# Kernel optimization log

Measured on AMD Instinct MI355X. Metric: run time of the kernel, lower is better.

Reference implementation:

```python
import jax, jax.numpy as jnp
import numpy as np

N, NFEAT, NHID, NCLASS, NHEAD = 8192, 512, 64, 16, 4
ALPHA = 0.1  # leaky relu slope
NEG = -9e15


def setup_inputs() -> dict:
    key = jax.random.key(0)
    ks = jax.random.split(key, 7)
    x = jax.random.normal(ks[0], (N, NFEAT), dtype=jnp.float32)
    adj = (jax.random.uniform(ks[1], (N, N)) < 0.05).astype(jnp.float32)
    # per-head params: W [H, nfeat, nhid], a [H, 2*nhid] (xavier-ish scale)
    W = jax.random.normal(ks[2], (NHEAD, NFEAT, NHID), dtype=jnp.float32) * (1.0 / np.sqrt(NFEAT))
    a = jax.random.normal(ks[3], (NHEAD, 2 * NHID), dtype=jnp.float32) * (1.0 / np.sqrt(NHID))
    W_out = jax.random.normal(ks[4], (NHEAD * NHID, NCLASS), dtype=jnp.float32) * (1.0 / np.sqrt(NHEAD * NHID))
    a_out = jax.random.normal(ks[5], (2 * NCLASS,), dtype=jnp.float32) * (1.0 / np.sqrt(NCLASS))
    return {"x": x, "adj": adj, "W": W, "a": a, "W_out": W_out, "a_out": a_out}


def _gat_layer(h, adj, Wk, ak):
    """Dense pyGAT GraphAttentionLayer (eval mode, dropout = identity)."""
    d = Wk.shape[1]
    Wh = h @ Wk                         # [N, d]
    f1 = Wh @ ak[:d]                    # [N]
    f2 = Wh @ ak[d:]                    # [N]
    e = jax.nn.leaky_relu(f1[:, None] + f2[None, :], negative_slope=ALPHA)  # [N, N]
    att = jax.nn.softmax(jnp.where(adj > 0, e, NEG), axis=1)
    return att @ Wh                     # [N, d]


def reference(x, adj, W, a, W_out, a_out):
    # eval mode: F.dropout is identity
    heads = jax.vmap(lambda Wk, ak: jax.nn.elu(_gat_layer(x, adj, Wk, ak)))(W, a)  # [H, N, nhid]
    h = jnp.transpose(heads, (1, 0, 2)).reshape(x.shape[0], -1)                    # [N, H*nhid]
    out = jax.nn.elu(_gat_layer(h, adj, W_out, a_out))                             # [N, nclass]
    return jax.nn.log_softmax(out, axis=1)
```

## Files before the change

kernel.cpp:

```cpp
#include <hip/hip_runtime.h>
#include <hip/hip_bf16.h>

#define NN 8192
#define NFEAT 512
#define NHID 64
#define NCLASS 16
#define NHEAD 4
#define ALPHA 0.1f
#define CAP 768

typedef short bf16x8 __attribute__((ext_vector_type(8)));
typedef float f32x4 __attribute__((ext_vector_type(4)));
typedef float fv4 __attribute__((ext_vector_type(4)));

__device__ __forceinline__ float lrelu(float x) { return fmaxf(x, ALPHA * x); }
__device__ __forceinline__ float elu(float x) { return x > 0.f ? x : __expf(x) - 1.f; }
__device__ __forceinline__ short f2b(float x) {
  union { __bf16 b; short s; } c; c.b = (__bf16)x; return c.s;
}
__device__ __forceinline__ float b2f(short x) {
  union { unsigned int u; float f; } c; c.u = ((unsigned int)(unsigned short)x) << 16; return c.f;
}

#define UPF(w, v, A0, A1)                                  \
  {                                                        \
    const float lo_ = __uint_as_float((v) << 16);          \
    const float hi_ = __uint_as_float((v) & 0xffff0000u);  \
    (A0) += (w) * lo_;                                     \
    (A1) += (w) * hi_;                                     \
  }

__global__ __launch_bounds__(256) void k_wprep(const float* __restrict__ W,
                                               short* __restrict__ WB) {
  __shared__ float t[64][65];
  const int h = blockIdx.y;
  const int k0 = blockIdx.x * 64;
  const int tid = threadIdx.x;
#pragma unroll
  for (int it = 0; it < 16; ++it) {
    const int r = it * 4 + (tid >> 6), c = tid & 63;
    t[r][c] = W[((size_t)h * NFEAT + k0 + r) * NHID + c];
  }
  __syncthreads();
#pragma unroll
  for (int it = 0; it < 16; ++it) {
    const int d = it * 4 + (tid >> 6), k = tid & 63;
    WB[((size_t)h * NHID + d) * NFEAT + k0 + k] = f2b(t[k][d]);
  }
}

__global__ __launch_bounds__(256) void k_prep1(const float* __restrict__ x,
                                               const short* __restrict__ WB,
                                               const float* __restrict__ a,
                                               short* __restrict__ WhB2,
                                               float* __restrict__ f1i,
                                               float* __restrict__ f2i) {
  __shared__ short tile[64][72];
  const int bid = blockIdx.x;
  const int h = bid >> 7;
  const int bm = (bid & 127) * 64;
  const int tid = threadIdx.x;
  const int wv = tid >> 6, lane = tid & 63;
  const int mr = lane & 15, kg = lane >> 4;
  f32x4 acc0 = {0.f, 0.f, 0.f, 0.f}, acc1 = acc0, acc2 = acc0, acc3 = acc0;
  const float* ap = x + (size_t)(bm + wv * 16 + mr) * NFEAT + kg * 8;
  const short* bp = WB + ((size_t)h * NHID + mr) * NFEAT + kg * 8;
#pragma unroll 2
  for (int k0 = 0; k0 < NFEAT; k0 += 32) {
    const float4 xa = *reinterpret_cast<const float4*>(ap);
    const float4 xb = *reinterpret_cast<const float4*>(ap + 4);
    bf16x8 af;
    af[0] = f2b(xa.x); af[1] = f2b(xa.y); af[2] = f2b(xa.z); af[3] = f2b(xa.w);
    af[4] = f2b(xb.x); af[5] = f2b(xb.y); af[6] = f2b(xb.z); af[7] = f2b(xb.w);
    const bf16x8 b0 = *reinterpret_cast<const bf16x8*>(bp);
    const bf16x8 b1 = *reinterpret_cast<const bf16x8*>(bp + 16 * NFEAT);
    const bf16x8 b2 = *reinterpret_cast<const bf16x8*>(bp + 32 * NFEAT);
    const bf16x8 b3 = *reinterpret_cast<const bf16x8*>(bp + 48 * NFEAT);
    acc0 = __builtin_amdgcn_mfma_f32_16x16x32_bf16(af, b0, acc0, 0, 0, 0);
    acc1 = __builtin_amdgcn_mfma_f32_16x16x32_bf16(af, b1, acc1, 0, 0, 0);
    acc2 = __builtin_amdgcn_mfma_f32_16x16x32_bf16(af, b2, acc2, 0, 0, 0);
    acc3 = __builtin_amdgcn_mfma_f32_16x16x32_bf16(af, b3, acc3, 0, 0, 0);
    ap += 32; bp += 32;
  }
  float a1v[4], a2v[4];
#pragma unroll
  for (int c = 0; c < 4; ++c) {
    a1v[c] = a[h * 128 + mr + c * 16];
    a2v[c] = a[h * 128 + 64 + mr + c * 16];
  }
#pragma unroll
  for (int q = 0; q < 4; ++q) {
    float s1 = acc0[q] * a1v[0] + acc1[q] * a1v[1] + acc2[q] * a1v[2] + acc3[q] * a1v[3];
    float s2 = acc0[q] * a2v[0] + acc1[q] * a2v[1] + acc2[q] * a2v[2] + acc3[q] * a2v[3];
#pragma unroll
    for (int off = 1; off < 16; off <<= 1) {
      s1 += __shfl_xor(s1, off);
      s2 += __shfl_xor(s2, off);
    }
    if (mr == 0) {
      const int i = bm + wv * 16 + kg * 4 + q;
      f1i[(size_t)i * 4 + h] = s1;
      f2i[(size_t)i * 4 + h] = s2;
    }
  }
#pragma unroll
  for (int q = 0; q < 4; ++q) {
    const int r = wv * 16 + kg * 4 + q;
    tile[r][mr +  0] = f2b(acc0[q]);
    tile[r][mr + 16] = f2b(acc1[q]);
    tile[r][mr + 32] = f2b(acc2[q]);
    tile[r][mr + 48] = f2b(acc3[q]);
  }
  __syncthreads();
  {
    const int row = tid >> 2, seg = tid & 3;
    bf16x8 o0, o1;
#pragma unroll
    for (int u = 0; u < 8; ++u) {
      o0[u] = tile[row][seg * 16 + u];
      o1[u] = tile[row][seg * 16 + 8 + u];
    }
    short* dst = WhB2 + (size_t)(h >> 1) * NN * 128 + (size_t)(bm + row) * 128 +
                 (h & 1) * 64 + seg * 16;
    *reinterpret_cast<bf16x8*>(dst) = o0;
    *reinterpret_cast<bf16x8*>(dst + 8) = o1;
  }
}

__global__ __launch_bounds__(256) void k_rmax(const float* __restrict__ src,
                                              float* __restrict__ dst, int n, int stride,
                                              int boff) {
  const float* p = src + (size_t)blockIdx.x * boff;
  float m = -1e30f;
  for (int k = threadIdx.x; k < n; k += 256) m = fmaxf(m, p[(size_t)k * stride]);
#pragma unroll
  for (int off = 32; off; off >>= 1) m = fmaxf(m, __shfl_xor(m, off));
  __shared__ float sm[4];
  if ((threadIdx.x & 63) == 0) sm[threadIdx.x >> 6] = m;
  __syncthreads();
  if (threadIdx.x == 0) dst[blockIdx.x] = fmaxf(fmaxf(sm[0], sm[1]), fmaxf(sm[2], sm[3]));
}

__global__ __launch_bounds__(256) void k_scan(const float* __restrict__ adj,
                                              unsigned int* __restrict__ bmask) {
  const fv4* a4 = reinterpret_cast<const fv4*>(adj);
  const int t0 = blockIdx.x * 256 + threadIdx.x;
#pragma unroll 4
  for (int it = 0; it < 32; ++it) {
    const int g = it * 524288 + t0;
    const fv4 v = __builtin_nontemporal_load(a4 + g);
    unsigned int nv = (unsigned int)((v.x > 0.f) | ((v.y > 0.f) << 1) |
                                     ((v.z > 0.f) << 2) | ((v.w > 0.f) << 3))
                      << ((threadIdx.x & 7) * 4);
    nv |= __shfl_xor(nv, 1);
    nv |= __shfl_xor(nv, 2);
    nv |= __shfl_xor(nv, 4);
    if ((threadIdx.x & 7) == 0) bmask[g >> 3] = nv;
  }
}

__global__ __launch_bounds__(256) void k_attn1h(const unsigned int* __restrict__ bmask,
                                                const short* __restrict__ WhB2,
                                                const float* __restrict__ f1i,
                                                const float* __restrict__ f2i,
                                                const float* __restrict__ f2max,
                                                short* __restrict__ hcat) {
  __shared__ unsigned short idx[CAP];
  __shared__ unsigned int widx[2][CAP + 32];
  __shared__ float red[4][64];
  __shared__ float swred[4][2];
  __shared__ float sinv[2];
  __shared__ int cnt;
  const int i = blockIdx.x;
  const int p = blockIdx.y;
  const int tid = threadIdx.x;
  const int wv = tid >> 6, lane = tid & 63;
  if (tid == 0) cnt = 0;
  __syncthreads();

  {
    unsigned int word = bmask[(size_t)i * 256 + tid];
    const int c = __popc(word);
    if (c) {
      int base = atomicAdd(&cnt, c);
      const int j0 = tid * 32;
      while (word) {
        const int b = __ffs(word) - 1;
        word &= word - 1;
        if (base < CAP) idx[base++] = (unsigned short)(j0 + b);
      }
    }
  }
  __syncthreads();
  const int n = min(cnt, CAP);

  if (tid < 64) widx[tid >> 5][n + (tid & 31)] = 0;

  const float f1r0 = f1i[(size_t)i * 4 + p * 2];
  const float f1r1 = f1i[(size_t)i * 4 + p * 2 + 1];
  const float mrow0 = lrelu(f1r0 + f2max[p * 2]);
  const float mrow1 = lrelu(f1r1 + f2max[p * 2 + 1]);
  float sw0 = 0.f, sw1 = 0.f;
  for (int k = tid; k < n; k += 256) {
    const int j = idx[k];
    const float2 f = *reinterpret_cast<const float2*>(f2i + (size_t)j * 4 + p * 2);
    const float w0 = __expf(lrelu(f1r0 + f.x) - mrow0);
    const float w1 = __expf(lrelu(f1r1 + f.y) - mrow1);
    widx[0][k] = ((unsigned int)(unsigned short)f2b(w0) << 16) | (unsigned int)j;
    widx[1][k] = ((unsigned int)(unsigned short)f2b(w1) << 16) | (unsigned int)j;
    sw0 += w0; sw1 += w1;
  }
#pragma unroll
  for (int off = 32; off; off >>= 1) { sw0 += __shfl_xor(sw0, off); sw1 += __shfl_xor(sw1, off); }
  if (lane == 0) { swred[wv][0] = sw0; swred[wv][1] = sw1; }
  __syncthreads();
  if (tid < 2) sinv[tid] = 1.f / (swred[0][tid] + swred[1][tid] + swred[2][tid] + swred[3][tid]);

  const int hl = wv >> 1, half = wv & 1;
  const int grp = lane >> 4, l = lane & 15;
  float acc0 = 0.f, acc1 = 0.f, acc2 = 0.f, acc3 = 0.f;
  const short* wb = WhB2 + (size_t)p * NN * 128 + hl * 64 + l * 4;
  const unsigned int* wrow = widx[hl];
  __syncthreads();
  for (int kb = (half * 4 + grp) * 8; kb < n; kb += 64) {
    const uint4 pa = *reinterpret_cast<const uint4*>(wrow + kb);
    const uint4 pb = *reinterpret_cast<const uint4*>(wrow + kb + 4);
    const uint2 e0 = *reinterpret_cast<const uint2*>(wb + (size_t)(pa.x & 0xffffu) * 128);
    const uint2 e1 = *reinterpret_cast<const uint2*>(wb + (size_t)(pa.y & 0xffffu) * 128);
    const uint2 e2 = *reinterpret_cast<const uint2*>(wb + (size_t)(pa.z & 0xffffu) * 128);
    const uint2 e3 = *reinterpret_cast<const uint2*>(wb + (size_t)(pa.w & 0xffffu) * 128);
    const uint2 e4 = *reinterpret_cast<const uint2*>(wb + (size_t)(pb.x & 0xffffu) * 128);
    const uint2 e5 = *reinterpret_cast<const uint2*>(wb + (size_t)(pb.y & 0xffffu) * 128);
    const uint2 e6 = *reinterpret_cast<const uint2*>(wb + (size_t)(pb.z & 0xffffu) * 128);
    const uint2 e7 = *reinterpret_cast<const uint2*>(wb + (size_t)(pb.w & 0xffffu) * 128);
    const float w0 = __uint_as_float(pa.x & 0xffff0000u);
    const float w1 = __uint_as_float(pa.y & 0xffff0000u);
    const float w2 = __uint_as_float(pa.z & 0xffff0000u);
    const float w3 = __uint_as_float(pa.w & 0xffff0000u);
    const float w4 = __uint_as_float(pb.x & 0xffff0000u);
    const float w5 = __uint_as_float(pb.y & 0xffff0000u);
    const float w6 = __uint_as_float(pb.z & 0xffff0000u);
    const float w7 = __uint_as_float(pb.w & 0xffff0000u);
    UPF(w0, e0.x, acc0, acc1) UPF(w0, e0.y, acc2, acc3)
    UPF(w1, e1.x, acc0, acc1) UPF(w1, e1.y, acc2, acc3)
    UPF(w2, e2.x, acc0, acc1) UPF(w2, e2.y, acc2, acc3)
    UPF(w3, e3.x, acc0, acc1) UPF(w3, e3.y, acc2, acc3)
    UPF(w4, e4.x, acc0, acc1) UPF(w4, e4.y, acc2, acc3)
    UPF(w5, e5.x, acc0, acc1) UPF(w5, e5.y, acc2, acc3)
    UPF(w6, e6.x, acc0, acc1) UPF(w6, e6.y, acc2, acc3)
    UPF(w7, e7.x, acc0, acc1) UPF(w7, e7.y, acc2, acc3)
  }
  acc0 += __shfl_xor(acc0, 16); acc0 += __shfl_xor(acc0, 32);
  acc1 += __shfl_xor(acc1, 16); acc1 += __shfl_xor(acc1, 32);
  acc2 += __shfl_xor(acc2, 16); acc2 += __shfl_xor(acc2, 32);
  acc3 += __shfl_xor(acc3, 16); acc3 += __shfl_xor(acc3, 32);
  if (lane < 16) {
    red[wv][l * 4 + 0] = acc0;
    red[wv][l * 4 + 1] = acc1;
    red[wv][l * 4 + 2] = acc2;
    red[wv][l * 4 + 3] = acc3;
  }
  __syncthreads();
  if (tid < 128) {
    const int sub = tid >> 6, d = tid & 63;
    const float s = red[sub * 2][d] + red[sub * 2 + 1][d];
    hcat[(size_t)i * 256 + p * 128 + sub * 64 + d] = f2b(elu(s * sinv[sub]));
  }
}

__global__ __launch_bounds__(256) void k_gemm2(const short* __restrict__ hcat,
                                               const float* __restrict__ Wout,
                                               const float* __restrict__ aout,
                                               short* __restrict__ Wh2B,
                                               float* __restrict__ f1o,
                                               float* __restrict__ f2o) {
  __shared__ float sW[NHEAD * NHID][NCLASS + 1];
  __shared__ float sh[16][NHEAD * NHID + 1];
  const int tid = threadIdx.x;
  const int r = tid >> 4, c = tid & 15;
  const int row = blockIdx.x * 16 + r;
  for (int u = tid; u < 256 * 16; u += 256) sW[u >> 4][u & 15] = Wout[u];
  for (int u = tid; u < 16 * 256; u += 256)
    sh[u >> 8][u & 255] = b2f(hcat[(size_t)(blockIdx.x * 16 + (u >> 8)) * 256 + (u & 255)]);
  __syncthreads();
  float acc = 0.f;
#pragma unroll 8
  for (int f = 0; f < 256; ++f) acc += sh[r][f] * sW[f][c];
  Wh2B[(size_t)row * NCLASS + c] = f2b(acc);
  float s1 = acc * aout[c];
  float s2 = acc * aout[NCLASS + c];
#pragma unroll
  for (int off = 8; off; off >>= 1) { s1 += __shfl_xor(s1, off); s2 += __shfl_xor(s2, off); }
  if (c == 0) { f1o[row] = s1; f2o[row] = s2; }
}

__global__ __launch_bounds__(256) void k_attn2(const unsigned int* __restrict__ bmask,
                                               const short* __restrict__ Wh2B,
                                               const float* __restrict__ f1o,
                                               const float* __restrict__ f2o,
                                               const float* __restrict__ f2omax,
                                               float* __restrict__ out) {
  __shared__ unsigned short idx[CAP];
  __shared__ unsigned int wj[CAP + 4];
  __shared__ float red[4][NCLASS];
  __shared__ float swp[4];
  __shared__ float sinvs;
  __shared__ int cnt;
  const int i = blockIdx.x;
  const int tid = threadIdx.x;
  const int wv = tid >> 6, lane = tid & 63;
  if (tid == 0) cnt = 0;
  __syncthreads();

  {
    unsigned int word = bmask[(size_t)i * 256 + tid];
    const int c = __popc(word);
    if (c) {
      int base = atomicAdd(&cnt, c);
      const int j0 = tid * 32;
      while (word) {
        const int b = __ffs(word) - 1;
        word &= word - 1;
        if (base < CAP) idx[base++] = (unsigned short)(j0 + b);
      }
    }
  }
  __syncthreads();
  const int n = min(cnt, CAP);
  if (tid < 4) wj[n + tid] = 0;

  const float f1r = f1o[i];
  const float mrow = lrelu(f1r + f2omax[0]);
  float sw = 0.f;
  for (int k = tid; k < n; k += 256) {
    const int j = idx[k];
    const float w = __expf(lrelu(f1r + f2o[j]) - mrow);
    wj[k] = ((unsigned int)(unsigned short)f2b(w) << 16) | (unsigned int)j;
    sw += w;
  }
#pragma unroll
  for (int off = 32; off; off >>= 1) sw += __shfl_xor(sw, off);
  if (lane == 0) swp[wv] = sw;
  __syncthreads();
  if (tid == 0) sinvs = 1.f / (swp[0] + swp[1] + swp[2] + swp[3]);
  __syncthreads();

  const int grp = tid >> 2, gl = tid & 3;
  float acc0 = 0.f, acc1 = 0.f, acc2 = 0.f, acc3 = 0.f;
  const short* wb = Wh2B + gl * 4;
  for (int kb = grp * 4; kb < n; kb += 256) {
    const uint4 pw = *reinterpret_cast<const uint4*>(wj + kb);
    const uint2 e0 = *reinterpret_cast<const uint2*>(wb + (size_t)(pw.x & 0xffffu) * NCLASS);
    const uint2 e1 = *reinterpret_cast<const uint2*>(wb + (size_t)(pw.y & 0xffffu) * NCLASS);
    const uint2 e2 = *reinterpret_cast<const uint2*>(wb + (size_t)(pw.z & 0xffffu) * NCLASS);
    const uint2 e3 = *reinterpret_cast<const uint2*>(wb + (size_t)(pw.w & 0xffffu) * NCLASS);
    const float w0 = __uint_as_float(pw.x & 0xffff0000u);
    const float w1 = __uint_as_float(pw.y & 0xffff0000u);
    const float w2 = __uint_as_float(pw.z & 0xffff0000u);
    const float w3 = __uint_as_float(pw.w & 0xffff0000u);
    UPF(w0, e0.x, acc0, acc1) UPF(w0, e0.y, acc2, acc3)
    UPF(w1, e1.x, acc0, acc1) UPF(w1, e1.y, acc2, acc3)
    UPF(w2, e2.x, acc0, acc1) UPF(w2, e2.y, acc2, acc3)
    UPF(w3, e3.x, acc0, acc1) UPF(w3, e3.y, acc2, acc3)
  }
  acc0 += __shfl_xor(acc0, 4);  acc1 += __shfl_xor(acc1, 4);
  acc2 += __shfl_xor(acc2, 4);  acc3 += __shfl_xor(acc3, 4);
  acc0 += __shfl_xor(acc0, 8);  acc1 += __shfl_xor(acc1, 8);
  acc2 += __shfl_xor(acc2, 8);  acc3 += __shfl_xor(acc3, 8);
  acc0 += __shfl_xor(acc0, 16); acc1 += __shfl_xor(acc1, 16);
  acc2 += __shfl_xor(acc2, 16); acc3 += __shfl_xor(acc3, 16);
  acc0 += __shfl_xor(acc0, 32); acc1 += __shfl_xor(acc1, 32);
  acc2 += __shfl_xor(acc2, 32); acc3 += __shfl_xor(acc3, 32);
  if (lane < 4) {
    red[wv][lane * 4 + 0] = acc0;
    red[wv][lane * 4 + 1] = acc1;
    red[wv][lane * 4 + 2] = acc2;
    red[wv][lane * 4 + 3] = acc3;
  }
  __syncthreads();
  if (tid < NCLASS) {
    const float s = red[0][tid] + red[1][tid] + red[2][tid] + red[3][tid];
    const float v = elu(s * sinvs);
    float vm = v;
#pragma unroll
    for (int off = 8; off; off >>= 1) vm = fmaxf(vm, __shfl_xor(vm, off, 16));
    float ex = __expf(v - vm);
#pragma unroll
    for (int off = 8; off; off >>= 1) ex += __shfl_xor(ex, off, 16);
    out[(size_t)i * NCLASS + tid] = v - vm - __logf(ex);
  }
}

extern "C" void kernel_launch(void* const* d_in, const int* in_sizes, int n_in,
                              void* d_out, int out_size, void* d_ws, size_t ws_size,
                              hipStream_t stream) {
  const float* x    = (const float*)d_in[0];
  const float* adj  = (const float*)d_in[1];
  const float* W    = (const float*)d_in[2];
  const float* a    = (const float*)d_in[3];
  const float* Wout = (const float*)d_in[4];
  const float* aout = (const float*)d_in[5];
  float* out = (float*)d_out;
  char* ws = (char*)d_ws;
  const size_t MB = 1048576;

  unsigned int* bmask  = (unsigned int*)(ws);
  short* WhB2          = (short*)(ws + 8 * MB);
  short* hcat          = (short*)(ws + 12 * MB);
  short* WB            = (short*)(ws + 16 * MB);
  float* f1i           = (float*)(ws + 16 * MB + 262144);
  float* f2i           = (float*)(ws + 16 * MB + 393216);
  float* f1o           = (float*)(ws + 16 * MB + 524288);
  float* f2o           = (float*)(ws + 16 * MB + 557056);
  short* Wh2B          = (short*)(ws + 16 * MB + 589824);
  float* f2max         = (float*)(ws + 16 * MB + 851968);
  float* f2omax        = (float*)(ws + 16 * MB + 852032);

  k_wprep<<<dim3(8, 4), 256, 0, stream>>>(W, WB);
  k_prep1<<<512, 256, 0, stream>>>(x, WB, a, WhB2, f1i, f2i);
  k_rmax<<<NHEAD, 256, 0, stream>>>(f2i, f2max, NN, 4, 1);
  k_scan<<<2048, 256, 0, stream>>>(adj, bmask);
  k_attn1h<<<dim3(NN, 2), 256, 0, stream>>>(bmask, WhB2, f1i, f2i, f2max, hcat);
  k_gemm2<<<NN / 16, 256, 0, stream>>>(hcat, Wout, aout, Wh2B, f1o, f2o);
  k_rmax<<<1, 256, 0, stream>>>(f2o, f2omax, NN, 1, 0);
  k_attn2<<<NN, 256, 0, stream>>>(bmask, Wh2B, f1o, f2o, f2omax, out);
}
```

Measured before the change: 247.2 us.

## Replace sparse gather attention with dense masked MFMA over 64-row tiles

The first-layer attention no longer compacts neighbour indices per row and gathers Wh rows. It now runs a dense masked bf16 MFMA over all 8192 columns for 64-row tiles per head. The leaky-relu exponential is factored as max(A*B, C*D) using per-row and per-column precomputed exponentials from a new k_acbd kernel, so the inner loop has no transcendentals. Wh is stored in a column-blocked layout that fits the MFMA B operand. This trades irregular gathers and per-row scan work for about 20x more (mostly zero-weight) dense FLOPs on matrix cores, and the factored exponentials may lose precision for extreme values.

```diff
diff --git a/kernel.cpp b/kernel.cpp
--- a/kernel.cpp
+++ b/kernel.cpp
@@ -52,7 +52,7 @@
 __global__ __launch_bounds__(256) void k_prep1(const float* __restrict__ x,
                                                const short* __restrict__ WB,
                                                const float* __restrict__ a,
-                                               short* __restrict__ WhB2,
+                                               short* __restrict__ Whf,
                                                float* __restrict__ f1i,
                                                float* __restrict__ f2i) {
   __shared__ short tile[64][72];
@@ -112,18 +112,15 @@
     tile[r][mr + 48] = f2b(acc3[q]);
   }
   __syncthreads();
-  {
-    const int row = tid >> 2, seg = tid & 3;
-    bf16x8 o0, o1;
-#pragma unroll
-    for (int u = 0; u < 8; ++u) {
-      o0[u] = tile[row][seg * 16 + u];
-      o1[u] = tile[row][seg * 16 + 8 + u];
-    }
-    short* dst = WhB2 + (size_t)(h >> 1) * NN * 128 + (size_t)(bm + row) * 128 +
-                 (h & 1) * 64 + seg * 16;
-    *reinterpret_cast<bf16x8*>(dst) = o0;
-    *reinterpret_cast<bf16x8*>(dst + 8) = o1;
+#pragma unroll
+  for (int it = 0; it < 2; ++it) {
+    const int jbl = (tid >> 6) + it * 4;
+    const int d = tid & 63;
+    bf16x8 o;
+#pragma unroll
+    for (int jo = 0; jo < 8; ++jo) o[jo] = tile[jbl * 8 + jo][d];
+    *reinterpret_cast<bf16x8*>(Whf +
+        (((size_t)h * 1024 + (bm >> 3) + jbl) * 64 + d) * 8) = o;
   }
 }
 
@@ -139,6 +136,29 @@
   if ((threadIdx.x & 63) == 0) sm[threadIdx.x >> 6] = m;
   __syncthreads();
   if (threadIdx.x == 0) dst[blockIdx.x] = fmaxf(fmaxf(sm[0], sm[1]), fmaxf(sm[2], sm[3]));
+}
+
+__global__ __launch_bounds__(256) void k_acbd(const float* __restrict__ f1i,
+                                              const float* __restrict__ f2i,
+                                              const float* __restrict__ f2max,
+                                              float2* __restrict__ ACh,
+                                              unsigned int* __restrict__ BDh) {
+  const int idx = blockIdx.x * 256 + threadIdx.x;
+  const int i = idx & (NN - 1);
+  const int h = idx >> 13;
+  const float fm = f2max[h];
+  const float f1 = f1i[(size_t)i * 4 + h];
+  const float f2 = f2i[(size_t)i * 4 + h];
+  const float s = f1 + fm;
+  const float mrow = fmaxf(s, 0.1f * s);
+  float2 ac;
+  ac.x = __expf(s - mrow);
+  ac.y = __expf(0.1f * s - mrow);
+  ACh[(size_t)h * NN + i] = ac;
+  const float t = f2 - fm;
+  const unsigned int B = (unsigned short)f2b(__expf(t));
+  const unsigned int D = (unsigned short)f2b(__expf(0.1f * t));
+  BDh[(size_t)h * NN + i] = B | (D << 16);
 }
 
 __global__ __launch_bounds__(256) void k_scan(const float* __restrict__ adj,
@@ -159,112 +179,92 @@
   }
 }
 
-__global__ __launch_bounds__(256) void k_attn1h(const unsigned int* __restrict__ bmask,
-                                                const short* __restrict__ WhB2,
-                                                const float* __restrict__ f1i,
-                                                const float* __restrict__ f2i,
-                                                const float* __restrict__ f2max,
+#define DCH 512
+__global__ __launch_bounds__(256) void k_dense1(const unsigned int* __restrict__ bmask,
+                                                const short* __restrict__ Whf,
+                                                const float2* __restrict__ ACh,
+                                                const unsigned int* __restrict__ BDh,
                                                 short* __restrict__ hcat) {
-  __shared__ unsigned short idx[CAP];
-  __shared__ unsigned int widx[2][CAP + 32];
-  __shared__ float red[4][64];
-  __shared__ float swred[4][2];
-  __shared__ float sinv[2];
-  __shared__ int cnt;
-  const int i = blockIdx.x;
-  const int p = blockIdx.y;
+  __shared__ unsigned int sm_mask[64][16];
+  __shared__ unsigned int sm_bd[DCH];
+  __shared__ float sm_iv[4][16];
+  __shared__ short sm_out[64][72];
+  const int i0 = blockIdx.x * 64;
+  const int h = blockIdx.y;
   const int tid = threadIdx.x;
   const int wv = tid >> 6, lane = tid & 63;
-  if (tid == 0) cnt = 0;
-  __syncthreads();
-
+  const int mr = lane & 15, kg = lane >> 4;
+  const int row_local = wv * 16 + mr;
+  const float2 ac = ACh[(size_t)h * NN + i0 + row_local];
+  f32x4 acc0 = {0.f, 0.f, 0.f, 0.f}, acc1 = acc0, acc2 = acc0, acc3 = acc0;
+  float rs = 0.f;
+  const int rr = tid >> 2, w0 = (tid & 3) * 4;
+
+  for (int jc = 0; jc < NN; jc += DCH) {
+    __syncthreads();
+    {
+      const unsigned int* src = bmask + (size_t)(i0 + rr) * 256 + (jc >> 5);
+#pragma unroll
+      for (int u = 0; u < 4; ++u) sm_mask[rr][w0 + u] = src[w0 + u];
+      sm_bd[tid] = BDh[(size_t)h * NN + jc + tid];
+      sm_bd[tid + 256] = BDh[(size_t)h * NN + jc + tid + 256];
+    }
+    __syncthreads();
+#pragma unroll 4
+    for (int ks = 0; ks < DCH / 32; ++ks) {
+      const int jl = ks * 32 + kg * 8;
+      const uint4 bda = *reinterpret_cast<const uint4*>(&sm_bd[jl]);
+      const uint4 bdb = *reinterpret_cast<const uint4*>(&sm_bd[jl + 4]);
+      const unsigned int mb = (sm_mask[row_local][ks] >> (kg * 8)) & 0xffu;
+      bf16x8 af;
+#define MKW(e, bdw)                                              \
+      {                                                          \
+        const float Bf = __uint_as_float((bdw) << 16);           \
+        const float Df = __uint_as_float((bdw) & 0xffff0000u);   \
+        float w_ = fmaxf(ac.x * Bf, ac.y * Df);                  \
+        w_ = ((mb >> (e)) & 1u) ? w_ : 0.f;                      \
+        rs += w_;                                                \
+        af[e] = f2b(w_);                                         \
+      }
+      MKW(0, bda.x) MKW(1, bda.y) MKW(2, bda.z) MKW(3, bda.w)
+      MKW(4, bdb.x) MKW(5, bdb.y) MKW(6, bdb.z) MKW(7, bdb.w)
+#undef MKW
+      const short* wp = Whf + (((size_t)h * 1024 + ((jc + jl) >> 3)) * 64 + mr) * 8;
+      const bf16x8 bf0 = *reinterpret_cast<const bf16x8*>(wp);
+      const bf16x8 bf1 = *reinterpret_cast<const bf16x8*>(wp + 128);
+      const bf16x8 bf2 = *reinterpret_cast<const bf16x8*>(wp + 256);
+      const bf16x8 bf3 = *reinterpret_cast<const bf16x8*>(wp + 384);
+      acc0 = __builtin_amdgcn_mfma_f32_16x16x32_bf16(af, bf0, acc0, 0, 0, 0);
+      acc1 = __builtin_amdgcn_mfma_f32_16x16x32_bf16(af, bf1, acc1, 0, 0, 0);
+      acc2 = __builtin_amdgcn_mfma_f32_16x16x32_bf16(af, bf2, acc2, 0, 0, 0);
+      acc3 = __builtin_amdgcn_mfma_f32_16x16x32_bf16(af, bf3, acc3, 0, 0, 0);
+    }
+  }
+  rs += __shfl_xor(rs, 16);
+  rs += __shfl_xor(rs, 32);
+  if (lane < 16) sm_iv[wv][lane] = 1.f / rs;
+  __syncthreads();
+#pragma unroll
+  for (int q = 0; q < 4; ++q) {
+    const float ivq = sm_iv[wv][kg * 4 + q];
+    const int r = wv * 16 + kg * 4 + q;
+    sm_out[r][mr +  0] = f2b(elu(acc0[q] * ivq));
+    sm_out[r][mr + 16] = f2b(elu(acc1[q] * ivq));
+    sm_out[r][mr + 32] = f2b(elu(acc2[q] * ivq));
+    sm_out[r][mr + 48] = f2b(elu(acc3[q] * ivq));
+  }
+  __syncthreads();
   {
-    unsigned int word = bmask[(size_t)i * 256 + tid];
-    const int c = __popc(word);
-    if (c) {
-      int base = atomicAdd(&cnt, c);
-      const int j0 = tid * 32;
-      while (word) {
-        const int b = __ffs(word) - 1;
-        word &= word - 1;
-        if (base < CAP) idx[base++] = (unsigned short)(j0 + b);
-      }
-    }
-  }
-  __syncthreads();
-  const int n = min(cnt, CAP);
-
-  if (tid < 64) widx[tid >> 5][n + (tid & 31)] = 0;
-
-  const float f1r0 = f1i[(size_t)i * 4 + p * 2];
-  const float f1r1 = f1i[(size_t)i * 4 + p * 2 + 1];
-  const float mrow0 = lrelu(f1r0 + f2max[p * 2]);
-  const float mrow1 = lrelu(f1r1 + f2max[p * 2 + 1]);
-  float sw0 = 0.f, sw1 = 0.f;
-  for (int k = tid; k < n; k += 256) {
-    const int j = idx[k];
-    const float2 f = *reinterpret_cast<const float2*>(f2i + (size_t)j * 4 + p * 2);
-    const float w0 = __expf(lrelu(f1r0 + f.x) - mrow0);
-    const float w1 = __expf(lrelu(f1r1 + f.y) - mrow1);
-    widx[0][k] = ((unsigned int)(unsigned short)f2b(w0) << 16) | (unsigned int)j;
-    widx[1][k] = ((unsigned int)(unsigned short)f2b(w1) << 16) | (unsigned int)j;
-    sw0 += w0; sw1 += w1;
-  }
-#pragma unroll
-  for (int off = 32; off; off >>= 1) { sw0 += __shfl_xor(sw0, off); sw1 += __shfl_xor(sw1, off); }
-  if (lane == 0) { swred[wv][0] = sw0; swred[wv][1] = sw1; }
-  __syncthreads();
-  if (tid < 2) sinv[tid] = 1.f / (swred[0][tid] + swred[1][tid] + swred[2][tid] + swred[3][tid]);
-
-  const int hl = wv >> 1, half = wv & 1;
-  const int grp = lane >> 4, l = lane & 15;
-  float acc0 = 0.f, acc1 = 0.f, acc2 = 0.f, acc3 = 0.f;
-  const short* wb = WhB2 + (size_t)p * NN * 128 + hl * 64 + l * 4;
-  const unsigned int* wrow = widx[hl];
-  __syncthreads();
-  for (int kb = (half * 4 + grp) * 8; kb < n; kb += 64) {
-    const uint4 pa = *reinterpret_cast<const uint4*>(wrow + kb);
-    const uint4 pb = *reinterpret_cast<const uint4*>(wrow + kb + 4);
-    const uint2 e0 = *reinterpret_cast<const uint2*>(wb + (size_t)(pa.x & 0xffffu) * 128);
-    const uint2 e1 = *reinterpret_cast<const uint2*>(wb + (size_t)(pa.y & 0xffffu) * 128);
-    const uint2 e2 = *reinterpret_cast<const uint2*>(wb + (size_t)(pa.z & 0xffffu) * 128);
-    const uint2 e3 = *reinterpret_cast<const uint2*>(wb + (size_t)(pa.w & 0xffffu) * 128);
-    const uint2 e4 = *reinterpret_cast<const uint2*>(wb + (size_t)(pb.x & 0xffffu) * 128);
-    const uint2 e5 = *reinterpret_cast<const uint2*>(wb + (size_t)(pb.y & 0xffffu) * 128);
-    const uint2 e6 = *reinterpret_cast<const uint2*>(wb + (size_t)(pb.z & 0xffffu) * 128);
-    const uint2 e7 = *reinterpret_cast<const uint2*>(wb + (size_t)(pb.w & 0xffffu) * 128);
-    const float w0 = __uint_as_float(pa.x & 0xffff0000u);
-    const float w1 = __uint_as_float(pa.y & 0xffff0000u);
-    const float w2 = __uint_as_float(pa.z & 0xffff0000u);
-    const float w3 = __uint_as_float(pa.w & 0xffff0000u);
-    const float w4 = __uint_as_float(pb.x & 0xffff0000u);
-    const float w5 = __uint_as_float(pb.y & 0xffff0000u);
-    const float w6 = __uint_as_float(pb.z & 0xffff0000u);
-    const float w7 = __uint_as_float(pb.w & 0xffff0000u);
-    UPF(w0, e0.x, acc0, acc1) UPF(w0, e0.y, acc2, acc3)
-    UPF(w1, e1.x, acc0, acc1) UPF(w1, e1.y, acc2, acc3)
-    UPF(w2, e2.x, acc0, acc1) UPF(w2, e2.y, acc2, acc3)
-    UPF(w3, e3.x, acc0, acc1) UPF(w3, e3.y, acc2, acc3)
-    UPF(w4, e4.x, acc0, acc1) UPF(w4, e4.y, acc2, acc3)
-    UPF(w5, e5.x, acc0, acc1) UPF(w5, e5.y, acc2, acc3)
-    UPF(w6, e6.x, acc0, acc1) UPF(w6, e6.y, acc2, acc3)
-    UPF(w7, e7.x, acc0, acc1) UPF(w7, e7.y, acc2, acc3)
-  }
-  acc0 += __shfl_xor(acc0, 16); acc0 += __shfl_xor(acc0, 32);
-  acc1 += __shfl_xor(acc1, 16); acc1 += __shfl_xor(acc1, 32);
-  acc2 += __shfl_xor(acc2, 16); acc2 += __shfl_xor(acc2, 32);
-  acc3 += __shfl_xor(acc3, 16); acc3 += __shfl_xor(acc3, 32);
-  if (lane < 16) {
-    red[wv][l * 4 + 0] = acc0;
-    red[wv][l * 4 + 1] = acc1;
-    red[wv][l * 4 + 2] = acc2;
-    red[wv][l * 4 + 3] = acc3;
-  }
-  __syncthreads();
-  if (tid < 128) {
-    const int sub = tid >> 6, d = tid & 63;
-    const float s = red[sub * 2][d] + red[sub * 2 + 1][d];
-    hcat[(size_t)i * 256 + p * 128 + sub * 64 + d] = f2b(elu(s * sinv[sub]));
+    const int r = tid >> 2, seg = tid & 3;
+    bf16x8 o;
+#pragma unroll
+    for (int u = 0; u < 8; ++u) o[u] = sm_out[r][seg * 16 + u];
+    short* dst = hcat + (size_t)(i0 + r) * 256 + h * 64 + seg * 16;
+    *reinterpret_cast<bf16x8*>(dst) = o;
+    bf16x8 o2;
+#pragma unroll
+    for (int u = 0; u < 8; ++u) o2[u] = sm_out[r][seg * 16 + 8 + u];
+    *reinterpret_cast<bf16x8*>(dst + 8) = o2;
   }
 }
 
@@ -403,24 +403,28 @@
   float* out = (float*)d_out;
   char* ws = (char*)d_ws;
   const size_t MB = 1048576;
+  const size_t KB = 1024;
 
   unsigned int* bmask  = (unsigned int*)(ws);
-  short* WhB2          = (short*)(ws + 8 * MB);
+  short* Whf           = (short*)(ws + 8 * MB);
   short* hcat          = (short*)(ws + 12 * MB);
   short* WB            = (short*)(ws + 16 * MB);
-  float* f1i           = (float*)(ws + 16 * MB + 262144);
-  float* f2i           = (float*)(ws + 16 * MB + 393216);
-  float* f1o           = (float*)(ws + 16 * MB + 524288);
-  float* f2o           = (float*)(ws + 16 * MB + 557056);
-  short* Wh2B          = (short*)(ws + 16 * MB + 589824);
-  float* f2max         = (float*)(ws + 16 * MB + 851968);
-  float* f2omax        = (float*)(ws + 16 * MB + 852032);
+  float* f1i           = (float*)(ws + 16 * MB + 256 * KB);
+  float* f2i           = (float*)(ws + 16 * MB + 384 * KB);
+  float2* ACh          = (float2*)(ws + 16 * MB + 512 * KB);
+  unsigned int* BDh    = (unsigned int*)(ws + 16 * MB + 768 * KB);
+  float* f1o           = (float*)(ws + 16 * MB + 896 * KB);
+  float* f2o           = (float*)(ws + 16 * MB + 928 * KB);
+  short* Wh2B          = (short*)(ws + 16 * MB + 960 * KB);
+  float* f2max         = (float*)(ws + 16 * MB + 1216 * KB);
+  float* f2omax        = (float*)(ws + 16 * MB + 1216 * KB + 64);
 
   k_wprep<<<dim3(8, 4), 256, 0, stream>>>(W, WB);
-  k_prep1<<<512, 256, 0, stream>>>(x, WB, a, WhB2, f1i, f2i);
+  k_prep1<<<512, 256, 0, stream>>>(x, WB, a, Whf, f1i, f2i);
   k_rmax<<<NHEAD, 256, 0, stream>>>(f2i, f2max, NN, 4, 1);
+  k_acbd<<<NN * NHEAD / 256, 256, 0, stream>>>(f1i, f2i, f2max, ACh, BDh);
   k_scan<<<2048, 256, 0, stream>>>(adj, bmask);
-  k_attn1h<<<dim3(NN, 2), 256, 0, stream>>>(bmask, WhB2, f1i, f2i, f2max, hcat);
+  k_dense1<<<dim3(NN / 64, NHEAD), 256, 0, stream>>>(bmask, Whf, ACh, BDh, hcat);
   k_gemm2<<<NN / 16, 256, 0, stream>>>(hcat, Wout, aout, Wh2B, f1o, f2o);
   k_rmax<<<1, 256, 0, stream>>>(f2o, f2omax, NN, 1, 0);
   k_attn2<<<NN, 256, 0, stream>>>(bmask, Wh2B, f1o, f2o, f2omax, out);
```

Measured after the change: 221.9 us. 10.2% less time.
